# Performance work log

Measured on AMD Instinct MI355X. Metric: run time of the kernel, lower is better.

## Reference

```python
import jax, jax.numpy as jnp
import numpy as np

N, C, T, V = 32, 64, 512, 21
INTER = 16  # out_channels // coff_embedding(4)
EPS = 1e-5


def _build_A():
    # 21-joint skeleton, spatial strategy: [self(identity), inward, outward], column-normalized
    parents = [-1, 0, 1, 2, 3, 1, 5, 6, 1, 8, 9, 0, 11, 12, 13, 0, 15, 16, 17, 7, 10]
    inw = np.zeros((V, V), np.float32)
    for i, p in enumerate(parents):
        if p >= 0:
            inw[i, p] = 1.0

    def norm(a):
        d = a.sum(0)
        return a * np.where(d > 0, 1.0 / d, 0.0).astype(np.float32)

    I = np.eye(V, dtype=np.float32)
    return np.stack([norm(I), norm(inw), norm(inw.T)]).astype(np.float32)


def setup_inputs():
    key = jax.random.key(0)
    k = jax.random.split(key, 24)
    rn = lambda i, s: jax.random.normal(k[i], s, jnp.float32)
    A = jnp.asarray(_build_A())
    return dict(
        x=rn(0, (N, C, T, V)),
        A=A,
        bn1_gamma=1.0 + 0.1 * rn(1, (C * V,)),
        bn1_beta=0.1 * rn(2, (C * V,)),
        bn1_mean=0.05 * rn(3, (C * V,)),
        bn1_var=jnp.ones((C * V,), jnp.float32),
        PA=A,
        alpha=rn(4, (1,)),
        wa=0.05 * rn(5, (3, INTER, C)), ba=0.05 * rn(6, (3, INTER)),
        wb=0.05 * rn(7, (3, INTER, C)), bb=0.05 * rn(8, (3, INTER)),
        wd=0.05 * rn(9, (3, C, C)), bd=0.05 * rn(10, (3, C)),
        bn2_gamma=1.0 + 0.1 * rn(11, (C,)),
        bn2_beta=0.1 * rn(12, (C,)),
        bn2_mean=0.05 * rn(13, (C,)),
        bn2_var=jnp.ones((C,), jnp.float32),
        w_sa=0.05 * rn(14, (1, C, V)), b_sa=0.05 * rn(15, (1,)),
        w_ta=0.05 * rn(16, (1, C, 9)), b_ta=0.05 * rn(17, (1,)),
        w_fc1=0.05 * rn(18, (C // 2, C)), b_fc1=0.05 * rn(19, (C // 2,)),
        w_fc2=0.05 * rn(20, (C, C // 2)), b_fc2=0.05 * rn(21, (C,)),
    )


def _conv1d(z, w, b):
    pad = (w.shape[2] - 1) // 2
    y = jax.lax.conv_general_dilated(z, w, (1,), [(pad, pad)],
                                     dimension_numbers=('NCH', 'OIH', 'NCH'))
    return y + b[None, :, None]


def reference(x, A, bn1_gamma, bn1_beta, bn1_mean, bn1_var, PA, alpha,
              wa, ba, wb, bb, wd, bd, bn2_gamma, bn2_beta, bn2_mean, bn2_var,
              w_sa, b_sa, w_ta, b_ta, w_fc1, b_fc1, w_fc2, b_fc2):
    n, c, t, v = x.shape
    # data_bn: (N,C,T,V) -> (N,V,T,C) -> raw reshape (N,V*C,T), BN1d, back to (N,C,T,V)
    xb = x.transpose(0, 3, 2, 1).reshape(n, v * c, t)
    scale1 = (bn1_gamma / jnp.sqrt(bn1_var + EPS))
    xb = (xb - bn1_mean[None, :, None]) * scale1[None, :, None] + bn1_beta[None, :, None]
    xb = xb.reshape(n, v, c, t).transpose(0, 2, 3, 1)  # (N,C,T,V)

    e = wa.shape[1]
    # attention embeddings, vectorized over the 3 subsets (s)
    a1 = (jnp.einsum('nctv,sec->nsvet', xb, wa) + ba[None, :, None, :, None]).reshape(n, 3, v, e * t)
    a2 = (jnp.einsum('nctv,sec->nsetv', xb, wb) + bb[None, :, :, None, None]).reshape(n, 3, e * t, v)
    attn = jnp.tanh(jnp.matmul(a1, a2) / float(e * t))  # (N,3,V,V)
    adj = PA[None] + attn * alpha[0]
    # graph aggregation: (N,1,C*T,V) @ (N,3,V,V)
    xz = jnp.matmul(xb.reshape(n, 1, c * t, v), adj).reshape(n, 3, c, t, v)
    y = jnp.einsum('nsctv,soc->notv', xz, wd) + bd.sum(0)[None, :, None, None]

    scale2 = (bn2_gamma / jnp.sqrt(bn2_var + EPS))
    y = (y - bn2_mean[None, :, None, None]) * scale2[None, :, None, None] + bn2_beta[None, :, None, None]
    y = jax.nn.relu(y + xb)  # residual (in==out -> identity down)

    # spatial attention
    se = y.mean(2)  # (N,C,V)
    y = y * jax.nn.sigmoid(_conv1d(se, w_sa, b_sa))[:, :, None, :] + y
    # temporal attention
    se = y.mean(3)  # (N,C,T)
    y = y * jax.nn.sigmoid(_conv1d(se, w_ta, b_ta))[:, :, :, None] + y
    # channel attention
    se = y.mean((2, 3))  # (N,C)
    se2 = jax.nn.sigmoid(jax.nn.relu(se @ w_fc1.T + b_fc1) @ w_fc2.T + b_fc2)
    y = y * se2[:, :, None, None] + y
    return jax.nn.relu(y)
```

## Files before the change

### kernel.cpp

```cpp
#include <hip/hip_runtime.h>
#include <hip/hip_bf16.h>
#include <math.h>


#define Nn 32
#define Cc 64
#define Tt 512
#define Vv 21
#define VP 24
#define Ss 3
#define EPSf 1e-5f
#define NCHUNK 16
#define SVV (Ss*Vv*Vv)
#define KSTR 136

typedef __attribute__((ext_vector_type(8))) short short8;
typedef __attribute__((ext_vector_type(4))) float f32x4;

__device__ __forceinline__ float sigm(float x){ return 1.f/(1.f+expf(-x)); }
__device__ __forceinline__ float bf2f(unsigned short u){ return __uint_as_float((unsigned)u << 16); }
__device__ __forceinline__ unsigned short f2bf(float f){
    __hip_bfloat16 h = __float2bfloat16(f);
    return *reinterpret_cast<unsigned short*>(&h);
}

__global__ __launch_bounds__(256) void k_wdT(
    const float* __restrict__ wd, const float* __restrict__ bd,
    const float* __restrict__ g2, const float* __restrict__ b2,
    const float* __restrict__ mu2, const float* __restrict__ var2,
    const float* __restrict__ g1, const float* __restrict__ b1,
    const float* __restrict__ mu1, const float* __restrict__ var1,
    unsigned short* __restrict__ wdF, float4* __restrict__ bn2p,
    float2* __restrict__ bn1p, float* __restrict__ M1)
{
    int i = blockIdx.x*256 + threadIdx.x;
    if (i < 1536){
        int s  = i / 512;
        int w  = (i >> 7) & 3;
        int ks = (i >> 6) & 1;
        int l  = i & 63;
        int o  = 16*w + (l & 15);
        #pragma unroll
        for (int j = 0; j < 8; ++j){
            int c = 32*ks + 8*(l >> 4) + j;
            wdF[(size_t)i*8 + j] = f2bf(wd[(s*64 + o)*64 + c]);
        }
    }
    if (i < 64){
        float bsum = bd[i] + bd[64+i] + bd[128+i];
        float sc = g2[i]*rsqrtf(var2[i]+EPSf);
        bn2p[i] = make_float4(bsum, sc, mu2[i], b2[i]);
    }
    if (i < 1344){
        float sc = g1[i]*rsqrtf(var1[i]+EPSf);
        bn1p[i] = make_float2(sc, b1[i] - mu1[i]*sc);
    }
    for (int j = i; j < Nn*Cc*Vv; j += 1536)
        M1[j] = 0.f;
}

__global__ __launch_bounds__(256) void k_xb(
    const float* __restrict__ x,
    const float2* __restrict__ bn1p,
    unsigned short* __restrict__ xbT)
{
    const int c0 = blockIdx.x;
    const int n  = blockIdx.y;
    const int tid = threadIdx.x;
    __shared__ unsigned short brick16[512*32];

    const float* xs = x + (size_t)(n*64 + c0)*10752;
    for (int i = tid; i < 2688; i += 256){
        float4 d = *reinterpret_cast<const float4*>(xs + i*4);
        #pragma unroll
        for (int e = 0; e < 4; ++e){
            int f = i*4 + e;
            int t = f / 21;
            int v = f - t*21;
            brick16[t*32 + ((v + 8*(t>>6)) & 31)] = f2bf(((const float*)&d)[e]);
        }
    }
    __syncthreads();

    if (tid < 192){
        const int agl = tid & 7;
        const int vp  = tid >> 3;
        const bool valid = (vp < 21);
        float scr[8], ofr[8];
        #pragma unroll
        for (int da = 0; da < 8; ++da){
            if (valid){
                float2 p = bn1p[vp*64 + agl*8 + da];
                scr[da] = p.x; ofr[da] = p.y;
            } else { scr[da] = 0.f; ofr[da] = 0.f; }
        }
        unsigned short* ob = xbT + ((size_t)(n*512 + c0)*24 + vp)*64 + agl*8;
        #pragma unroll
        for (int m = 0; m < 8; ++m){
            unsigned short pk[8];
            #pragma unroll
            for (int da = 0; da < 8; ++da){
                int row = agl*64 + da*8 + m;
                float xv = bf2f(brick16[row*32 + ((vp + 8*agl) & 31)]);
                float r = xv*scr[da] + ofr[da];
                pk[da] = valid ? f2bf(r) : (unsigned short)0;
            }
            *reinterpret_cast<uint4*>(ob + (size_t)m*64*24*64) =
                *reinterpret_cast<const uint4*>(pk);
        }
    }
}

__global__ __launch_bounds__(256) void k_wab(
    const float* __restrict__ wa, const float* __restrict__ wb,
    unsigned short* __restrict__ wawbF)
{
    int i = blockIdx.x*256 + threadIdx.x;
    if (i >= 768) return;
    int mt = i / 128;
    int ks = (i / 64) & 1;
    int l  = i & 63;
    int e  = l & 15;
    int g  = l >> 4;
    const float* src = (mt < 3) ? wa : wb;
    int s = (mt < 3) ? mt : mt - 3;
    #pragma unroll
    for (int j = 0; j < 8; ++j){
        int c = ks*32 + 8*g + j;
        wawbF[(size_t)i*8 + j] = f2bf(src[(s*16 + e)*64 + c]);
    }
}

__global__ __launch_bounds__(256) void k_attn(
    const unsigned short* __restrict__ xbT,
    const unsigned short* __restrict__ wawbF,
    const float* __restrict__ ba, const float* __restrict__ bb,
    float* __restrict__ part)
{
    const int chunk = blockIdx.x;
    const int n = blockIdx.y;
    const int tid = threadIdx.x;
    const int w  = tid >> 6;
    const int l  = tid & 63;
    const int g  = l >> 4;
    const int ln = l & 15;

    __shared__ unsigned short m1buf[3*32*KSTR];
    __shared__ unsigned short m2buf[3*32*KSTR];

    for (int i = tid; i < 3*8*KSTR; i += 256){
        int s = i / (8*KSTR), r = i % (8*KSTR);
        int off = (s*32 + 24)*KSTR + r;
        m1buf[off] = 0; m2buf[off] = 0;
    }

    short8 aF[6][2];
    float4 bias4[6];
    #pragma unroll
    for (int mt = 0; mt < 6; ++mt){
        #pragma unroll
        for (int ks = 0; ks < 2; ++ks)
            aF[mt][ks] = *reinterpret_cast<const short8*>(wawbF + (size_t)((mt*2+ks)*64 + l)*8);
        const float* bsrc = (mt < 3) ? (ba + mt*16) : (bb + (mt-3)*16);
        bias4[mt] = *reinterpret_cast<const float4*>(bsrc + 4*g);
    }

    f32x4 accB[3];
    #pragma unroll
    for (int q = 0; q < 3; ++q) accB[q] = (f32x4){0.f,0.f,0.f,0.f};

    int colv[3], colt[3];
    #pragma unroll
    for (int q = 0; q < 3; ++q){
        int col = (3*w + q)*16 + ln;
        colt[q] = col / 24;
        colv[q] = col % 24;
    }

    for (int st = 0; st < 4; ++st){
        const int tb = chunk*32 + st*8;
        #pragma unroll
        for (int q = 0; q < 3; ++q){
            const unsigned short* bp = xbT + ((size_t)(n*512 + tb + colt[q])*24 + colv[q])*64;
            short8 b0 = *reinterpret_cast<const short8*>(bp + 8*g);
            short8 b1 = *reinterpret_cast<const short8*>(bp + 32 + 8*g);
            #pragma unroll
            for (int mt = 0; mt < 6; ++mt){
                f32x4 c;
                c[0] = bias4[mt].x; c[1] = bias4[mt].y;
                c[2] = bias4[mt].z; c[3] = bias4[mt].w;
                c = __builtin_amdgcn_mfma_f32_16x16x32_bf16(aF[mt][0], b0, c, 0, 0, 0);
                c = __builtin_amdgcn_mfma_f32_16x16x32_bf16(aF[mt][1], b1, c, 0, 0, 0);
                unsigned short* dst = (mt < 3) ? m1buf : m2buf;
                int s = (mt < 3) ? mt : mt - 3;
                unsigned u0 = (unsigned)f2bf(c[0]) | ((unsigned)f2bf(c[1]) << 16);
                unsigned u1 = (unsigned)f2bf(c[2]) | ((unsigned)f2bf(c[3]) << 16);
                int off = (s*32 + colv[q])*KSTR + colt[q]*16 + 4*g;
                *reinterpret_cast<uint2*>(dst + off) = make_uint2(u0, u1);
            }
        }
        __syncthreads();
        #pragma unroll
        for (int q = 0; q < 3; ++q){
            int ct = 3*w + q;
            int s = ct >> 2, mtile = (ct >> 1) & 1, ntile = ct & 1;
            #pragma unroll
            for (int kk = 0; kk < 4; ++kk){
                short8 a = *reinterpret_cast<const short8*>(&m1buf[(s*32 + mtile*16 + ln)*KSTR + kk*32 + 8*g]);
                short8 b = *reinterpret_cast<const short8*>(&m2buf[(s*32 + ntile*16 + ln)*KSTR + kk*32 + 8*g]);
                accB[q] = __builtin_amdgcn_mfma_f32_16x16x32_bf16(a, b, accB[q], 0, 0, 0);
            }
        }
        __syncthreads();
    }

    float* pout = part + (size_t)(n*NCHUNK + chunk)*SVV;
    #pragma unroll
    for (int q = 0; q < 3; ++q){
        int ct = 3*w + q;
        int s = ct >> 2, mtile = (ct >> 1) & 1, ntile = ct & 1;
        int v = ntile*16 + ln;
        #pragma unroll
        for (int r = 0; r < 4; ++r){
            int u = mtile*16 + 4*g + r;
            if (u < 21 && v < 21)
                pout[s*441 + u*21 + v] = accB[q][r];
        }
    }
}

__global__ void k_adj(const float* __restrict__ part, const float* __restrict__ PA,
                      const float* __restrict__ alpha, float* __restrict__ adj)
{
    int i = blockIdx.x*256 + threadIdx.x;
    if (i >= Nn*SVV) return;
    int n = i / SVV;
    int idx = i % SVV;
    float pre = 0.f;
    for (int ch = 0; ch < NCHUNK; ++ch)
        pre += part[(size_t)(n*NCHUNK+ch)*SVV + idx];
    adj[i] = PA[idx] + tanhf(pre * (1.f/8192.f)) * alpha[0];
}

__global__ __launch_bounds__(256) void k_adjF(const float* __restrict__ adj,
                                              unsigned short* __restrict__ adjF)
{
    int i = blockIdx.x*256 + threadIdx.x;
    if (i >= Nn*Ss*2*64) return;
    int n = i / 384;
    int r = i % 384;
    int s = r / 128;
    int r2 = r % 128;
    int h = r2 >> 6;
    int l = r2 & 63;
    int v = 16*h + (l & 15);
    #pragma unroll
    for (int j = 0; j < 8; ++j){
        int u = 8*(l >> 4) + j;
        float val = (u < 21 && v < 21) ? adj[(size_t)n*SVV + s*441 + u*21 + v] : 0.f;
        adjF[(size_t)i*8 + j] = f2bf(val);
    }
}

__global__ __launch_bounds__(256) void k_y0(
    const unsigned short* __restrict__ xbT,
    const unsigned short* __restrict__ adjF,
    const unsigned short* __restrict__ wdF,
    const float4* __restrict__ bn2p,
    float* __restrict__ y0, float* __restrict__ M1)
{
    const int n  = blockIdx.y;
    const int t0 = blockIdx.x * 4;
    const int tid = threadIdx.x;
    const int w  = tid >> 6;
    const int l  = tid & 63;
    const int g  = l >> 4;
    const int ln = l & 15;

    __shared__ unsigned short xbuf[64*136];
    __shared__ unsigned short zbuf[128*72];

    {
        int c = tid >> 2, t = tid & 3;
        *reinterpret_cast<uint4*>(&xbuf[c*136 + t*32 + 24]) = make_uint4(0u,0u,0u,0u);
    }
    for (int k = 0; k < 3; ++k){
        int i = tid + k*256;
        int u = i % 24, t = (i/24) & 3, cg = i / 96;
        uint4 d = *reinterpret_cast<const uint4*>(
            xbT + ((size_t)(n*512 + t0 + t)*24 + u)*64 + cg*8);
        const unsigned short* p = reinterpret_cast<const unsigned short*>(&d);
        #pragma unroll
        for (int dc = 0; dc < 8; ++dc)
            xbuf[(cg*8 + dc)*136 + t*32 + u] = p[dc];
    }
    __syncthreads();

    short8 ax[4];
    #pragma unroll
    for (int t = 0; t < 4; ++t)
        ax[t] = *reinterpret_cast<const short8*>(&xbuf[(16*w + ln)*136 + t*32 + 8*g]);

    short8 badj[3][2];
    {
        const unsigned short* ap = adjF + (size_t)n*Ss*2*64*8;
        #pragma unroll
        for (int s = 0; s < 3; ++s)
            #pragma unroll
            for (int h = 0; h < 2; ++h)
                badj[s][h] = *reinterpret_cast<const short8*>(ap + ((s*2 + h)*64 + l)*8);
    }

    f32x4 acc[8];
    #pragma unroll
    for (int ct = 0; ct < 8; ++ct) acc[ct] = (f32x4){0.f,0.f,0.f,0.f};

    for (int s = 0; s < 3; ++s){
        if (s) __syncthreads();
        f32x4 dz[8];
        #pragma unroll
        for (int ct = 0; ct < 8; ++ct)
            dz[ct] = __builtin_amdgcn_mfma_f32_16x16x32_bf16(
                         ax[ct>>1], badj[s][ct&1], (f32x4){0.f,0.f,0.f,0.f}, 0, 0, 0);
        #pragma unroll
        for (int ct = 0; ct < 8; ++ct){
            unsigned u0 = (unsigned)f2bf(dz[ct][0]) | ((unsigned)f2bf(dz[ct][1]) << 16);
            unsigned u1 = (unsigned)f2bf(dz[ct][2]) | ((unsigned)f2bf(dz[ct][3]) << 16);
            int col = (ct >> 1)*32 + (ct & 1)*16 + ln;
            *reinterpret_cast<uint2*>(&zbuf[col*72 + 16*w + 4*g]) = make_uint2(u0, u1);
        }
        __syncthreads();
        short8 aw0 = *reinterpret_cast<const short8*>(wdF + (size_t)(((s*4 + w)*2 + 0)*64 + l)*8);
        short8 aw1 = *reinterpret_cast<const short8*>(wdF + (size_t)(((s*4 + w)*2 + 1)*64 + l)*8);
        #pragma unroll
        for (int ct = 0; ct < 8; ++ct){
            int col = (ct >> 1)*32 + (ct & 1)*16 + ln;
            short8 b0 = *reinterpret_cast<const short8*>(&zbuf[col*72 + 0  + 8*g]);
            short8 b1 = *reinterpret_cast<const short8*>(&zbuf[col*72 + 32 + 8*g]);
            acc[ct] = __builtin_amdgcn_mfma_f32_16x16x32_bf16(aw0, b0, acc[ct], 0, 0, 0);
            acc[ct] = __builtin_amdgcn_mfma_f32_16x16x32_bf16(aw1, b1, acc[ct], 0, 0, 0);
        }
    }

    float4 bp[4];
    #pragma unroll
    for (int r = 0; r < 4; ++r) bp[r] = bn2p[16*w + 4*g + r];
    float m1a[4][2];
    #pragma unroll
    for (int r = 0; r < 4; ++r){ m1a[r][0] = 0.f; m1a[r][1] = 0.f; }
    #pragma unroll
    for (int ct = 0; ct < 8; ++ct){
        const int t  = ct >> 1;
        const int h  = ct & 1;
        const int vp = h*16 + ln;
        if (vp < 21){
            #pragma unroll
            for (int r = 0; r < 4; ++r){
                const int o = 16*w + 4*g + r;
                float val = acc[ct][r] + bp[r].x;
                val = (val - bp[r].z)*bp[r].y + bp[r].w;
                val += bf2f(xbuf[o*136 + t*32 + vp]);
                val = fmaxf(val, 0.f);
                y0[((size_t)(n*64 + o)*512 + t0 + t)*21 + vp] = val;
                m1a[r][h] += val;
            }
        }
    }
    #pragma unroll
    for (int h = 0; h < 2; ++h){
        const int vp = h*16 + ln;
        if (vp < 21){
            #pragma unroll
            for (int r = 0; r < 4; ++r){
                const int o = 16*w + 4*g + r;
                atomicAdd(&M1[n*1344 + o*21 + vp], m1a[r][h]);
            }
        }
    }
}

__global__ __launch_bounds__(256) void k_s1(const float* __restrict__ M1, const float* __restrict__ w_sa,
                     const float* __restrict__ b_sa, float* __restrict__ s1)
{
    const int n = blockIdx.x, tid = threadIdx.x;
    __shared__ float m1s[64][22];
    __shared__ float ws[64][22];
    __shared__ float red[12][21];
    for (int i = tid; i < 1344; i += 256){
        int c = i / 21, v = i % 21;
        m1s[c][v] = M1[(size_t)(n*64+c)*21 + v];
        ws[c][v]  = w_sa[i];
    }
    __syncthreads();
    const int v = tid % 21;
    const int cg = tid / 21;
    float sum = 0.f;
    if (tid < 252){
        for (int c = cg; c < 64; c += 12){
            #pragma unroll
            for (int k = 0; k < 21; ++k){
                int src = v + k - 10;
                if (src >= 0 && src < 21)
                    sum += m1s[c][src] * ws[c][k];
            }
        }
        red[cg][v] = sum;
    }
    __syncthreads();
    if (tid < 21){
        float tot = b_sa[0];
        #pragma unroll
        for (int g = 0; g < 12; ++g) tot += red[g][tid] * (1.f/512.f);
        s1[n*Vv + tid] = 1.f + sigm(tot);
    }
}

__global__ __launch_bounds__(256) void k_M2(const float* __restrict__ y0, const float* __restrict__ s1,
                      float* __restrict__ M2)
{
    int t = blockIdx.x*256 + threadIdx.x;
    int nc = blockIdx.y;
    int n = nc >> 6;
    __shared__ float s1s[21];
    if (threadIdx.x < 21) s1s[threadIdx.x] = s1[n*Vv + threadIdx.x];
    __syncthreads();
    const float* p = &y0[ ((size_t)nc*Tt + t)*Vv ];
    float sum = 0.f;
    #pragma unroll
    for (int v = 0; v < 21; ++v) sum += p[v]*s1s[v];
    M2[(size_t)nc*Tt + t] = sum;
}

__global__ __launch_bounds__(256) void k_s2(const float* __restrict__ M2, const float* __restrict__ w_ta,
                      const float* __restrict__ b_ta, float* __restrict__ s2)
{
    const int n = blockIdx.y;
    const int t0 = blockIdx.x * 64;
    const int tid = threadIdx.x;
    __shared__ float m2s[64][72];
    __shared__ float wts[576];
    __shared__ float red[4][64];
    for (int i = tid; i < 64*72; i += 256){
        int c = i / 72, tt = i % 72;
        int src = t0 + tt - 4;
        m2s[c][tt] = (src >= 0 && src < 512) ? M2[(size_t)(n*64+c)*512 + src] : 0.f;
    }
    for (int i = tid; i < 576; i += 256) wts[i] = w_ta[i];
    __syncthreads();
    const int tl = tid & 63;
    const int cg = tid >> 6;
    float sum = 0.f;
    for (int c = cg*16; c < cg*16+16; ++c){
        #pragma unroll
        for (int k = 0; k < 9; ++k)
            sum += m2s[c][tl + k] * wts[c*9 + k];
    }
    red[cg][tl] = sum;
    __syncthreads();
    if (cg == 0){
        float tot = b_ta[0] + (red[0][tl]+red[1][tl]+red[2][tl]+red[3][tl]) * (1.f/21.f);
        s2[n*512 + t0 + tl] = 1.f + sigm(tot);
    }
}

__global__ __launch_bounds__(256) void k_sec(const float* __restrict__ M2, const float* __restrict__ s2,
                      float* __restrict__ sec)
{
    const int c = blockIdx.x, n = blockIdx.y, tid = threadIdx.x;
    const float* row = &M2[(size_t)(n*Cc+c)*Tt];
    const float* s2r = &s2[n*Tt];
    float acc = row[tid]*s2r[tid] + row[tid+256]*s2r[tid+256];
    #pragma unroll
    for (int off = 32; off > 0; off >>= 1)
        acc += __shfl_down(acc, off, 64);
    __shared__ float red[4];
    if ((tid & 63) == 0) red[tid >> 6] = acc;
    __syncthreads();
    if (tid == 0)
        sec[n*Cc + c] = (red[0]+red[1]+red[2]+red[3]) * (1.f/(512.f*21.f));
}

__global__ __launch_bounds__(64) void k_s3fc(const float* __restrict__ sec,
                     const float* __restrict__ w1, const float* __restrict__ bf1,
                     const float* __restrict__ w2, const float* __restrict__ bf2,
                     float* __restrict__ s3)
{
    int n = blockIdx.x, c = threadIdx.x;
    __shared__ float secs[64];
    __shared__ float hh[32];
    secs[c] = sec[n*Cc + c];
    __syncthreads();
    if (c < 32){
        float h = bf1[c];
        #pragma unroll 8
        for (int k = 0; k < 64; ++k) h += w1[c*64+k]*secs[k];
        hh[c] = fmaxf(h, 0.f);
    }
    __syncthreads();
    float o = bf2[c];
    #pragma unroll 8
    for (int k = 0; k < 32; ++k) o += w2[c*32+k]*hh[k];
    s3[n*Cc + c] = 1.f + sigm(o);
}

__global__ __launch_bounds__(256) void k_final(float* __restrict__ y,
    const float* __restrict__ s1, const float* __restrict__ s2, const float* __restrict__ s3)
{
    const int c = blockIdx.x, n = blockIdx.y, tid = threadIdx.x;
    __shared__ float s1s[21];
    __shared__ float s2s[512];
    if (tid < 21) s1s[tid] = s1[n*Vv + tid];
    for (int i = tid; i < 512; i += 256) s2s[i] = s2[n*512 + i];
    __syncthreads();
    const float sc3 = s3[n*Cc + c];
    float* base = y + (size_t)(n*Cc + c)*10752;
    for (int i = tid; i < 2688; i += 256){
        float4 d = *reinterpret_cast<const float4*>(base + i*4);
        float r[4];
        #pragma unroll
        for (int e = 0; e < 4; ++e){
            int f = i*4 + e;
            int t = f / 21;
            int v = f - t*21;
            r[e] = fmaxf(((const float*)&d)[e] * s1s[v] * s2s[t] * sc3, 0.f);
        }
        *reinterpret_cast<float4*>(base + i*4) = make_float4(r[0], r[1], r[2], r[3]);
    }
}

extern "C" void kernel_launch(void* const* d_in, const int* in_sizes, int n_in,
                              void* d_out, int out_size, void* d_ws, size_t ws_size,
                              hipStream_t stream)
{
    const float* x    = (const float*)d_in[0];
    const float* g1   = (const float*)d_in[2];
    const float* b1   = (const float*)d_in[3];
    const float* mu1  = (const float*)d_in[4];
    const float* var1 = (const float*)d_in[5];
    const float* PA   = (const float*)d_in[6];
    const float* alpha= (const float*)d_in[7];
    const float* wa   = (const float*)d_in[8];
    const float* ba   = (const float*)d_in[9];
    const float* wb   = (const float*)d_in[10];
    const float* bb   = (const float*)d_in[11];
    const float* wd   = (const float*)d_in[12];
    const float* bd   = (const float*)d_in[13];
    const float* g2   = (const float*)d_in[14];
    const float* b2   = (const float*)d_in[15];
    const float* mu2  = (const float*)d_in[16];
    const float* var2 = (const float*)d_in[17];
    const float* w_sa = (const float*)d_in[18];
    const float* b_sa = (const float*)d_in[19];
    const float* w_ta = (const float*)d_in[20];
    const float* b_ta = (const float*)d_in[21];
    const float* w_fc1= (const float*)d_in[22];
    const float* b_fc1= (const float*)d_in[23];
    const float* w_fc2= (const float*)d_in[24];
    const float* b_fc2= (const float*)d_in[25];

    unsigned short* xbT = (unsigned short*)d_ws;
    float* fws  = (float*)d_ws + 12582912;
    float* part = fws;
    float* adjw = part + 677376;
    float* M1   = adjw + 42336;
    float* s1   = M1   + 43008;
    float* M2   = s1   + 672;
    float* s2   = M2   + 1048576;
    float* s3   = s2   + 16384;
    float4* bn2p = (float4*)(s3 + 2048);
    unsigned short* wdF   = (unsigned short*)((float*)bn2p + 256);
    unsigned short* adjF  = wdF + 12288;
    unsigned short* wawbF = adjF + 98304;
    float* sec  = (float*)(wawbF + 6144);
    float2* bn1p = (float2*)(sec + 2048);
    float* y0   = (float*)d_out;

    k_wdT <<<6, 256, 0, stream>>>(wd, bd, g2, b2, mu2, var2, g1, b1, mu1, var1,
                                  wdF, bn2p, bn1p, M1);
    k_wab <<<3, 256, 0, stream>>>(wa, wb, wawbF);
    k_xb  <<<dim3(64, Nn), 256, 0, stream>>>(x, bn1p, xbT);
    k_attn<<<dim3(NCHUNK, Nn), 256, 0, stream>>>(xbT, wawbF, ba, bb, part);
    k_adj <<<(Nn*SVV + 255)/256, 256, 0, stream>>>(part, PA, alpha, adjw);
    k_adjF<<<48, 256, 0, stream>>>(adjw, adjF);
    k_y0  <<<dim3(Tt/4, Nn), 256, 0, stream>>>(xbT, adjF, wdF, bn2p, y0, M1);
    k_s1  <<<Nn, 256, 0, stream>>>(M1, w_sa, b_sa, s1);
    k_M2  <<<dim3(Tt/256, Nn*Cc), 256, 0, stream>>>(y0, s1, M2);
    k_s2  <<<dim3(8, Nn), 256, 0, stream>>>(M2, w_ta, b_ta, s2);
    k_sec <<<dim3(Cc, Nn), 256, 0, stream>>>(M2, s2, sec);
    k_s3fc<<<Nn, 64, 0, stream>>>(sec, w_fc1, b_fc1, w_fc2, b_fc2, s3);
    k_final<<<dim3(Cc, Nn), 256, 0, stream>>>(y0, s1, s2, s3);
}
```

Measured before the change: 194.0 us.

## Merge prep and adjacency kernels, loop k_y0 over time groups, replace atomics with partials

Merges the two weight-prep kernels into one and the adjacency reduce and bf16 packing kernels into one per-sample block that stages data in shared memory. k_y0 now processes four 4-step time groups per block (grid of 32 instead of 128 per sample), so the adjacency fragments and BN parameters are loaded once per 16 time steps. The M1 atomicAdds are replaced by per-block partial sums that a new reduction kernel adds up, which also removes the M1 zeroing. The aim is fewer kernel launches and less atomic traffic, at the cost of fewer blocks in k_y0 and one extra small kernel.

```diff
diff --git a/kernel.cpp b/kernel.cpp
--- a/kernel.cpp
+++ b/kernel.cpp
@@ -24,14 +24,15 @@
     return *reinterpret_cast<unsigned short*>(&h);
 }
 
-__global__ __launch_bounds__(256) void k_wdT(
+__global__ __launch_bounds__(256) void k_prep(
     const float* __restrict__ wd, const float* __restrict__ bd,
     const float* __restrict__ g2, const float* __restrict__ b2,
     const float* __restrict__ mu2, const float* __restrict__ var2,
     const float* __restrict__ g1, const float* __restrict__ b1,
     const float* __restrict__ mu1, const float* __restrict__ var1,
+    const float* __restrict__ wa, const float* __restrict__ wb,
     unsigned short* __restrict__ wdF, float4* __restrict__ bn2p,
-    float2* __restrict__ bn1p, float* __restrict__ M1)
+    float2* __restrict__ bn1p, unsigned short* __restrict__ wawbF)
 {
     int i = blockIdx.x*256 + threadIdx.x;
     if (i < 1536){
@@ -46,6 +47,20 @@
             wdF[(size_t)i*8 + j] = f2bf(wd[(s*64 + o)*64 + c]);
         }
     }
+    if (i < 768){
+        int mt = i / 128;
+        int ks = (i / 64) & 1;
+        int l  = i & 63;
+        int e  = l & 15;
+        int g  = l >> 4;
+        const float* src = (mt < 3) ? wa : wb;
+        int s = (mt < 3) ? mt : mt - 3;
+        #pragma unroll
+        for (int j = 0; j < 8; ++j){
+            int c = ks*32 + 8*g + j;
+            wawbF[(size_t)i*8 + j] = f2bf(src[(s*16 + e)*64 + c]);
+        }
+    }
     if (i < 64){
         float bsum = bd[i] + bd[64+i] + bd[128+i];
         float sc = g2[i]*rsqrtf(var2[i]+EPSf);
@@ -55,8 +70,6 @@
         float sc = g1[i]*rsqrtf(var1[i]+EPSf);
         bn1p[i] = make_float2(sc, b1[i] - mu1[i]*sc);
     }
-    for (int j = i; j < Nn*Cc*Vv; j += 1536)
-        M1[j] = 0.f;
 }
 
 __global__ __launch_bounds__(256) void k_xb(
@@ -108,26 +121,6 @@
             *reinterpret_cast<uint4*>(ob + (size_t)m*64*24*64) =
                 *reinterpret_cast<const uint4*>(pk);
         }
-    }
-}
-
-__global__ __launch_bounds__(256) void k_wab(
-    const float* __restrict__ wa, const float* __restrict__ wb,
-    unsigned short* __restrict__ wawbF)
-{
-    int i = blockIdx.x*256 + threadIdx.x;
-    if (i >= 768) return;
-    int mt = i / 128;
-    int ks = (i / 64) & 1;
-    int l  = i & 63;
-    int e  = l & 15;
-    int g  = l >> 4;
-    const float* src = (mt < 3) ? wa : wb;
-    int s = (mt < 3) ? mt : mt - 3;
-    #pragma unroll
-    for (int j = 0; j < 8; ++j){
-        int c = ks*32 + 8*g + j;
-        wawbF[(size_t)i*8 + j] = f2bf(src[(s*16 + e)*64 + c]);
     }
 }
 
@@ -229,36 +222,36 @@
     }
 }
 
-__global__ void k_adj(const float* __restrict__ part, const float* __restrict__ PA,
-                      const float* __restrict__ alpha, float* __restrict__ adj)
-{
-    int i = blockIdx.x*256 + threadIdx.x;
-    if (i >= Nn*SVV) return;
-    int n = i / SVV;
-    int idx = i % SVV;
-    float pre = 0.f;
-    for (int ch = 0; ch < NCHUNK; ++ch)
-        pre += part[(size_t)(n*NCHUNK+ch)*SVV + idx];
-    adj[i] = PA[idx] + tanhf(pre * (1.f/8192.f)) * alpha[0];
-}
-
-__global__ __launch_bounds__(256) void k_adjF(const float* __restrict__ adj,
-                                              unsigned short* __restrict__ adjF)
-{
-    int i = blockIdx.x*256 + threadIdx.x;
-    if (i >= Nn*Ss*2*64) return;
-    int n = i / 384;
-    int r = i % 384;
-    int s = r / 128;
-    int r2 = r % 128;
-    int h = r2 >> 6;
-    int l = r2 & 63;
-    int v = 16*h + (l & 15);
-    #pragma unroll
-    for (int j = 0; j < 8; ++j){
-        int u = 8*(l >> 4) + j;
-        float val = (u < 21 && v < 21) ? adj[(size_t)n*SVV + s*441 + u*21 + v] : 0.f;
-        adjF[(size_t)i*8 + j] = f2bf(val);
+__global__ __launch_bounds__(256) void k_adjB(
+    const float* __restrict__ part, const float* __restrict__ PA,
+    const float* __restrict__ alpha, unsigned short* __restrict__ adjF)
+{
+    const int n = blockIdx.x;
+    const int tid = threadIdx.x;
+    __shared__ float adjs[SVV];
+    const float al = alpha[0];
+    for (int idx = tid; idx < SVV; idx += 256){
+        float pre = 0.f;
+        #pragma unroll
+        for (int ch = 0; ch < NCHUNK; ++ch)
+            pre += part[(size_t)(n*NCHUNK+ch)*SVV + idx];
+        adjs[idx] = PA[idx] + tanhf(pre * (1.f/8192.f)) * al;
+    }
+    __syncthreads();
+    for (int i = tid; i < 384; i += 256){
+        int s = i / 128;
+        int h = (i >> 6) & 1;
+        int l = i & 63;
+        int v = 16*h + (l & 15);
+        unsigned short pk[8];
+        #pragma unroll
+        for (int j = 0; j < 8; ++j){
+            int u = 8*(l >> 4) + j;
+            float val = (u < 21 && v < 21) ? adjs[s*441 + u*21 + v] : 0.f;
+            pk[j] = f2bf(val);
+        }
+        *reinterpret_cast<uint4*>(adjF + ((size_t)n*384 + i)*8) =
+            *reinterpret_cast<const uint4*>(pk);
     }
 }
 
@@ -267,10 +260,10 @@
     const unsigned short* __restrict__ adjF,
     const unsigned short* __restrict__ wdF,
     const float4* __restrict__ bn2p,
-    float* __restrict__ y0, float* __restrict__ M1)
+    float* __restrict__ y0, float* __restrict__ M1P)
 {
     const int n  = blockIdx.y;
-    const int t0 = blockIdx.x * 4;
+    const int tb = blockIdx.x;
     const int tid = threadIdx.x;
     const int w  = tid >> 6;
     const int l  = tid & 63;
@@ -280,27 +273,6 @@
     __shared__ unsigned short xbuf[64*136];
     __shared__ unsigned short zbuf[128*72];
 
-    {
-        int c = tid >> 2, t = tid & 3;
-        *reinterpret_cast<uint4*>(&xbuf[c*136 + t*32 + 24]) = make_uint4(0u,0u,0u,0u);
-    }
-    for (int k = 0; k < 3; ++k){
-        int i = tid + k*256;
-        int u = i % 24, t = (i/24) & 3, cg = i / 96;
-        uint4 d = *reinterpret_cast<const uint4*>(
-            xbT + ((size_t)(n*512 + t0 + t)*24 + u)*64 + cg*8);
-        const unsigned short* p = reinterpret_cast<const unsigned short*>(&d);
-        #pragma unroll
-        for (int dc = 0; dc < 8; ++dc)
-            xbuf[(cg*8 + dc)*136 + t*32 + u] = p[dc];
-    }
-    __syncthreads();
-
-    short8 ax[4];
-    #pragma unroll
-    for (int t = 0; t < 4; ++t)
-        ax[t] = *reinterpret_cast<const short8*>(&xbuf[(16*w + ln)*136 + t*32 + 8*g]);
-
     short8 badj[3][2];
     {
         const unsigned short* ap = adjF + (size_t)n*Ss*2*64*8;
@@ -310,62 +282,89 @@
             for (int h = 0; h < 2; ++h)
                 badj[s][h] = *reinterpret_cast<const short8*>(ap + ((s*2 + h)*64 + l)*8);
     }
-
-    f32x4 acc[8];
-    #pragma unroll
-    for (int ct = 0; ct < 8; ++ct) acc[ct] = (f32x4){0.f,0.f,0.f,0.f};
-
-    for (int s = 0; s < 3; ++s){
-        if (s) __syncthreads();
-        f32x4 dz[8];
-        #pragma unroll
-        for (int ct = 0; ct < 8; ++ct)
-            dz[ct] = __builtin_amdgcn_mfma_f32_16x16x32_bf16(
-                         ax[ct>>1], badj[s][ct&1], (f32x4){0.f,0.f,0.f,0.f}, 0, 0, 0);
+    float4 bp[4];
+    #pragma unroll
+    for (int r = 0; r < 4; ++r) bp[r] = bn2p[16*w + 4*g + r];
+
+    float m1a[4][2];
+    #pragma unroll
+    for (int r = 0; r < 4; ++r){ m1a[r][0] = 0.f; m1a[r][1] = 0.f; }
+
+    for (int tg = 0; tg < 4; ++tg){
+        const int t0 = tb*16 + tg*4;
+        if (tg) __syncthreads();
+        {
+            int c = tid >> 2, t = tid & 3;
+            *reinterpret_cast<uint4*>(&xbuf[c*136 + t*32 + 24]) = make_uint4(0u,0u,0u,0u);
+        }
+        for (int k = 0; k < 3; ++k){
+            int i = tid + k*256;
+            int u = i % 24, t = (i/24) & 3, cg = i / 96;
+            uint4 d = *reinterpret_cast<const uint4*>(
+                xbT + ((size_t)(n*512 + t0 + t)*24 + u)*64 + cg*8);
+            const unsigned short* p = reinterpret_cast<const unsigned short*>(&d);
+            #pragma unroll
+            for (int dc = 0; dc < 8; ++dc)
+                xbuf[(cg*8 + dc)*136 + t*32 + u] = p[dc];
+        }
+        __syncthreads();
+
+        short8 ax[4];
+        #pragma unroll
+        for (int t = 0; t < 4; ++t)
+            ax[t] = *reinterpret_cast<const short8*>(&xbuf[(16*w + ln)*136 + t*32 + 8*g]);
+
+        f32x4 acc[8];
+        #pragma unroll
+        for (int ct = 0; ct < 8; ++ct) acc[ct] = (f32x4){0.f,0.f,0.f,0.f};
+
+        for (int s = 0; s < 3; ++s){
+            if (s) __syncthreads();
+            f32x4 dz[8];
+            #pragma unroll
+            for (int ct = 0; ct < 8; ++ct)
+                dz[ct] = __builtin_amdgcn_mfma_f32_16x16x32_bf16(
+                             ax[ct>>1], badj[s][ct&1], (f32x4){0.f,0.f,0.f,0.f}, 0, 0, 0);
+            #pragma unroll
+            for (int ct = 0; ct < 8; ++ct){
+                unsigned u0 = (unsigned)f2bf(dz[ct][0]) | ((unsigned)f2bf(dz[ct][1]) << 16);
+                unsigned u1 = (unsigned)f2bf(dz[ct][2]) | ((unsigned)f2bf(dz[ct][3]) << 16);
+                int col = (ct >> 1)*32 + (ct & 1)*16 + ln;
+                *reinterpret_cast<uint2*>(&zbuf[col*72 + 16*w + 4*g]) = make_uint2(u0, u1);
+            }
+            __syncthreads();
+            short8 aw0 = *reinterpret_cast<const short8*>(wdF + (size_t)(((s*4 + w)*2 + 0)*64 + l)*8);
+            short8 aw1 = *reinterpret_cast<const short8*>(wdF + (size_t)(((s*4 + w)*2 + 1)*64 + l)*8);
+            #pragma unroll
+            for (int ct = 0; ct < 8; ++ct){
+                int col = (ct >> 1)*32 + (ct & 1)*16 + ln;
+                short8 b0 = *reinterpret_cast<const short8*>(&zbuf[col*72 + 0  + 8*g]);
+                short8 b1 = *reinterpret_cast<const short8*>(&zbuf[col*72 + 32 + 8*g]);
+                acc[ct] = __builtin_amdgcn_mfma_f32_16x16x32_bf16(aw0, b0, acc[ct], 0, 0, 0);
+                acc[ct] = __builtin_amdgcn_mfma_f32_16x16x32_bf16(aw1, b1, acc[ct], 0, 0, 0);
+            }
+        }
+
         #pragma unroll
         for (int ct = 0; ct < 8; ++ct){
-            unsigned u0 = (unsigned)f2bf(dz[ct][0]) | ((unsigned)f2bf(dz[ct][1]) << 16);
-            unsigned u1 = (unsigned)f2bf(dz[ct][2]) | ((unsigned)f2bf(dz[ct][3]) << 16);
-            int col = (ct >> 1)*32 + (ct & 1)*16 + ln;
-            *reinterpret_cast<uint2*>(&zbuf[col*72 + 16*w + 4*g]) = make_uint2(u0, u1);
-        }
-        __syncthreads();
-        short8 aw0 = *reinterpret_cast<const short8*>(wdF + (size_t)(((s*4 + w)*2 + 0)*64 + l)*8);
-        short8 aw1 = *reinterpret_cast<const short8*>(wdF + (size_t)(((s*4 + w)*2 + 1)*64 + l)*8);
-        #pragma unroll
-        for (int ct = 0; ct < 8; ++ct){
-            int col = (ct >> 1)*32 + (ct & 1)*16 + ln;
-            short8 b0 = *reinterpret_cast<const short8*>(&zbuf[col*72 + 0  + 8*g]);
-            short8 b1 = *reinterpret_cast<const short8*>(&zbuf[col*72 + 32 + 8*g]);
-            acc[ct] = __builtin_amdgcn_mfma_f32_16x16x32_bf16(aw0, b0, acc[ct], 0, 0, 0);
-            acc[ct] = __builtin_amdgcn_mfma_f32_16x16x32_bf16(aw1, b1, acc[ct], 0, 0, 0);
-        }
-    }
-
-    float4 bp[4];
-    #pragma unroll
-    for (int r = 0; r < 4; ++r) bp[r] = bn2p[16*w + 4*g + r];
-    float m1a[4][2];
-    #pragma unroll
-    for (int r = 0; r < 4; ++r){ m1a[r][0] = 0.f; m1a[r][1] = 0.f; }
-    #pragma unroll
-    for (int ct = 0; ct < 8; ++ct){
-        const int t  = ct >> 1;
-        const int h  = ct & 1;
-        const int vp = h*16 + ln;
-        if (vp < 21){
-            #pragma unroll
-            for (int r = 0; r < 4; ++r){
-                const int o = 16*w + 4*g + r;
-                float val = acc[ct][r] + bp[r].x;
-                val = (val - bp[r].z)*bp[r].y + bp[r].w;
-                val += bf2f(xbuf[o*136 + t*32 + vp]);
-                val = fmaxf(val, 0.f);
-                y0[((size_t)(n*64 + o)*512 + t0 + t)*21 + vp] = val;
-                m1a[r][h] += val;
-            }
-        }
-    }
+            const int t  = ct >> 1;
+            const int h  = ct & 1;
+            const int vp = h*16 + ln;
+            if (vp < 21){
+                #pragma unroll
+                for (int r = 0; r < 4; ++r){
+                    const int o = 16*w + 4*g + r;
+                    float val = acc[ct][r] + bp[r].x;
+                    val = (val - bp[r].z)*bp[r].y + bp[r].w;
+                    val += bf2f(xbuf[o*136 + t*32 + vp]);
+                    val = fmaxf(val, 0.f);
+                    y0[((size_t)(n*64 + o)*512 + t0 + t)*21 + vp] = val;
+                    m1a[r][h] += val;
+                }
+            }
+        }
+    }
+
     #pragma unroll
     for (int h = 0; h < 2; ++h){
         const int vp = h*16 + ln;
@@ -373,9 +372,21 @@
             #pragma unroll
             for (int r = 0; r < 4; ++r){
                 const int o = 16*w + 4*g + r;
-                atomicAdd(&M1[n*1344 + o*21 + vp], m1a[r][h]);
-            }
-        }
+                M1P[((size_t)(n*32 + tb))*1344 + o*21 + vp] = m1a[r][h];
+            }
+        }
+    }
+}
+
+__global__ __launch_bounds__(256) void k_M1red(const float* __restrict__ M1P, float* __restrict__ M1)
+{
+    const int n = blockIdx.x, tid = threadIdx.x;
+    for (int j = tid; j < 1344; j += 256){
+        float s = 0.f;
+        #pragma unroll 8
+        for (int tb = 0; tb < 32; ++tb)
+            s += M1P[((size_t)(n*32 + tb))*1344 + j];
+        M1[n*1344 + j] = s;
     }
 }
 
@@ -388,7 +399,7 @@
     __shared__ float red[12][21];
     for (int i = tid; i < 1344; i += 256){
         int c = i / 21, v = i % 21;
-        m1s[c][v] = M1[(size_t)(n*64+c)*21 + v];
+        m1s[c][v] = M1[(size_t)n*1344 + i];
         ws[c][v]  = w_sa[i];
     }
     __syncthreads();
@@ -561,8 +572,7 @@
     unsigned short* xbT = (unsigned short*)d_ws;
     float* fws  = (float*)d_ws + 12582912;
     float* part = fws;
-    float* adjw = part + 677376;
-    float* M1   = adjw + 42336;
+    float* M1   = part + 677376;
     float* s1   = M1   + 43008;
     float* M2   = s1   + 672;
     float* s2   = M2   + 1048576;
@@ -573,16 +583,16 @@
     unsigned short* wawbF = adjF + 98304;
     float* sec  = (float*)(wawbF + 6144);
     float2* bn1p = (float2*)(sec + 2048);
+    float* M1P  = (float*)(bn1p + 1344);
     float* y0   = (float*)d_out;
 
-    k_wdT <<<6, 256, 0, stream>>>(wd, bd, g2, b2, mu2, var2, g1, b1, mu1, var1,
-                                  wdF, bn2p, bn1p, M1);
-    k_wab <<<3, 256, 0, stream>>>(wa, wb, wawbF);
+    k_prep<<<6, 256, 0, stream>>>(wd, bd, g2, b2, mu2, var2, g1, b1, mu1, var1,
+                                  wa, wb, wdF, bn2p, bn1p, wawbF);
     k_xb  <<<dim3(64, Nn), 256, 0, stream>>>(x, bn1p, xbT);
     k_attn<<<dim3(NCHUNK, Nn), 256, 0, stream>>>(xbT, wawbF, ba, bb, part);
-    k_adj <<<(Nn*SVV + 255)/256, 256, 0, stream>>>(part, PA, alpha, adjw);
-    k_adjF<<<48, 256, 0, stream>>>(adjw, adjF);
-    k_y0  <<<dim3(Tt/4, Nn), 256, 0, stream>>>(xbT, adjF, wdF, bn2p, y0, M1);
+    k_adjB<<<Nn, 256, 0, stream>>>(part, PA, alpha, adjF);
+    k_y0  <<<dim3(32, Nn), 256, 0, stream>>>(xbT, adjF, wdF, bn2p, y0, M1P);
+    k_M1red<<<Nn, 256, 0, stream>>>(M1P, M1);
     k_s1  <<<Nn, 256, 0, stream>>>(M1, w_sa, b_sa, s1);
     k_M2  <<<dim3(Tt/256, Nn*Cc), 256, 0, stream>>>(y0, s1, M2);
     k_s2  <<<dim3(8, Nn), 256, 0, stream>>>(M2, w_ta, b_ta, s2);
```

Result: faster. 171.4 us (-11.6%).
